# Optimization experiments

Measured on AMD Instinct MI355X. Metric: run time of the kernel, lower is better.

The kernel has to match this reference:

```python
import jax, jax.numpy as jnp
import numpy as np
import math

B, S, HID, H, DH = 4, 1024, 1024, 16, 64  # batch, seq, hidden, heads, head_dim


def _rotate_half(x):
    x1, x2 = jnp.split(x, 2, axis=-1)
    return jnp.concatenate([-x2, x1], axis=-1)


def _apply_rope(t, freqs):
    # t: [B,H,S,DH], freqs: [S,rot_dim]; here rot_dim == DH so no pass-through part
    rot = freqs.shape[-1]
    cos_ = jnp.cos(freqs)[None, None, :, :].astype(t.dtype)
    sin_ = jnp.sin(freqs)[None, None, :, :].astype(t.dtype)
    t_rot, t_pass = t[..., :rot], t[..., rot:]
    t_rot = t_rot * cos_ + _rotate_half(t_rot) * sin_
    return jnp.concatenate([t_rot, t_pass], axis=-1)


def setup_inputs() -> dict:
    key = jax.random.key(0)
    ks = jax.random.split(key, 8)
    hidden_states = jax.random.normal(ks[0], (B, S, HID), dtype=jnp.float32)
    # additive mask: valid prefix of random length per batch row, -1e9 on padding
    lengths = jax.random.randint(ks[1], (B,), 3 * S // 4, S + 1)
    pos = jnp.arange(S)
    attention_mask = jnp.where(pos[None, :] < lengths[:, None], 0.0, -1e9)
    attention_mask = attention_mask.astype(jnp.float32)[:, None, None, :]  # [B,1,1,S]
    # rotary frequencies: standard RoPE angles, duplicated halves -> [S, DH]
    inv_freq = 1.0 / (10000.0 ** (jnp.arange(0, DH // 2, dtype=jnp.float32) / (DH // 2)))
    ang = pos.astype(jnp.float32)[:, None] * inv_freq[None, :]
    freqs = jnp.concatenate([ang, ang], axis=-1)  # [S, DH]
    sc = 0.02
    Wq = jax.random.normal(ks[2], (HID, HID), dtype=jnp.float32) * sc
    Wk = jax.random.normal(ks[3], (HID, HID), dtype=jnp.float32) * sc
    Wv = jax.random.normal(ks[4], (HID, HID), dtype=jnp.float32) * sc
    bq = jnp.zeros((HID,), dtype=jnp.float32)
    bk = jnp.zeros((HID,), dtype=jnp.float32)
    bv = jnp.zeros((HID,), dtype=jnp.float32)
    return dict(hidden_states=hidden_states, attention_mask=attention_mask, freqs=freqs,
                Wq=Wq, bq=bq, Wk=Wk, bk=bk, Wv=Wv, bv=bv)


def reference(hidden_states, attention_mask, freqs, Wq, bq, Wk, bk, Wv, bv):
    b, s, _ = hidden_states.shape
    # QKV projections -> [B,H,S,DH]
    q = (hidden_states @ Wq + bq).reshape(b, s, H, DH).transpose(0, 2, 1, 3)
    k = (hidden_states @ Wk + bk).reshape(b, s, H, DH).transpose(0, 2, 1, 3)
    v = (hidden_states @ Wv + bv).reshape(b, s, H, DH).transpose(0, 2, 1, 3)
    # inline RoPE on q and k (same freqs for both, as (rotary_pos_emb,)*2)
    q = _apply_rope(q, freqs)
    k = _apply_rope(k, freqs)
    scores = jnp.einsum('bhqd,bhkd->bhqk', q, k) / math.sqrt(DH)
    scores = scores + attention_mask  # additive mask broadcast over [B,H,S,S]
    probs = jax.nn.softmax(scores, axis=-1)
    # no_prob_mask filtering: zero out masked key columns
    probs = jnp.where(attention_mask < -1e-5, 0.0, probs)
    # dropout prob is 0.0 (eval) -> identity
    ctx = jnp.einsum('bhqk,bhkd->bhqd', probs, v)
    ctx = ctx.transpose(0, 2, 1, 3).reshape(b, s, H * DH)
    return ctx
```

## Files before the change

### kernel.cpp

```cpp
#include <hip/hip_runtime.h>
#include <hip/hip_bf16.h>
#include <cmath>

#define NB   4
#define NS   1024
#define NHID 1024
#define NH   16
#define NDH  64
#define QKV_PLANE (NB * NH * NS * NDH)

typedef __attribute__((ext_vector_type(8))) short bf16x8;
typedef __attribute__((ext_vector_type(4))) float f32x4;
typedef __attribute__((ext_vector_type(8))) unsigned short u16x8;

typedef __attribute__((address_space(1))) const void gv_t;
typedef __attribute__((address_space(3))) void       lv_t;

__device__ __forceinline__ void gload16(const void* g, void* l) {
    __builtin_amdgcn_global_load_lds((gv_t*)g, (lv_t*)l, 16, 0, 0);
}

__device__ __forceinline__ unsigned short f2b(float f) {
    union { float f; unsigned int u; } v; v.f = f;
    unsigned int r = (v.u + 0x7fff + ((v.u >> 16) & 1)) >> 16;
    return (unsigned short)r;
}

__device__ __forceinline__ unsigned int f2b2(float a, float b) {
    __hip_bfloat162 h = __float22bfloat162_rn(make_float2(a, b));
    union { __hip_bfloat162 h; unsigned int u; } v; v.h = h;
    return v.u;
}

__device__ __forceinline__ float fexp2(float x) {
#if __has_builtin(__builtin_amdgcn_exp2f)
    return __builtin_amdgcn_exp2f(x);
#else
    return exp2f(x);
#endif
}

__global__ __launch_bounds__(256) void prep_kernel(
    const float* __restrict__ hs, const float* __restrict__ freqs,
    const float* __restrict__ Wq, const float* __restrict__ Wk,
    const float* __restrict__ Wv,
    unsigned short* __restrict__ hsb, unsigned short* __restrict__ wt,
    float2* __restrict__ cs)
{
    const int z   = blockIdx.z;
    const int tid = threadIdx.x;

    if (z == 3) {
        const int bx = blockIdx.y * 16 + blockIdx.x;
        #pragma unroll
        for (int c = 0; c < 16; ++c) {
            const int idx = bx * 16384 + (c * 256 + tid) * 4;
            float4 v = *(const float4*)&hs[idx];
            ushort4 o;
            o.x = f2b(v.x); o.y = f2b(v.y); o.z = f2b(v.z); o.w = f2b(v.w);
            *(ushort4*)&hsb[idx] = o;
        }
        return;
    }
    if (z == 4) {
        const int bx = blockIdx.y * 16 + blockIdx.x;
        if (bx < 128) {
            const int id = bx * 256 + tid;
            const int s = id >> 5, d = id & 31;
            const float ang = freqs[s * NDH + d];
            float sn, cn;
            sincosf(ang, &sn, &cn);
            cs[id] = make_float2(cn, sn);
        }
        return;
    }

    const float* __restrict__ W = (z == 0) ? Wq : (z == 1) ? Wk : Wv;
    __shared__ float t[64][65];
    const int k0 = blockIdx.x * 64, n0 = blockIdx.y * 64;
    #pragma unroll
    for (int c = 0; c < 16; ++c) {
        const int flat = c * 256 + tid;
        const int r = flat >> 6, cc = flat & 63;
        t[r][cc] = W[(size_t)(k0 + r) * NHID + n0 + cc];
    }
    __syncthreads();
    #pragma unroll
    for (int c = 0; c < 16; ++c) {
        const int flat = c * 256 + tid;
        const int r = flat >> 6, cc = flat & 63;
        wt[(size_t)(z * 1024 + n0 + r) * NHID + k0 + cc] = f2b(t[cc][r]);
    }
}

__global__ __launch_bounds__(256) void fused_gemm_kernel(
    const unsigned short* __restrict__ hsb,
    const unsigned short* __restrict__ wt,
    const float2* __restrict__ cs,
    const float* __restrict__ bq, const float* __restrict__ bk,
    const float* __restrict__ bv,
    unsigned short* __restrict__ qkv)
{
    __shared__ short SH[16896];
    short* As = SH;
    short* Bs = SH + 8192;

    const int tid  = threadIdx.x;
    const int lane = tid & 63;
    const int wv   = __builtin_amdgcn_readfirstlane(tid >> 6);
    const bool vmode = (blockIdx.x >= 16);

    const unsigned short* Amat;
    const unsigned short* Bmat;
    int a_base, b_base, m0, n0, vb_ = 0;
    if (!vmode) {
        n0 = blockIdx.x * 128;
        m0 = blockIdx.y * 128;
        Amat = hsb;  a_base = m0;
        Bmat = wt;   b_base = n0;
    } else {
        m0  = (blockIdx.x - 16) * 128;
        vb_ = blockIdx.y >> 3;
        n0  = (blockIdx.y & 7) * 128;
        Amat = wt;   a_base = 2048 + m0;
        Bmat = hsb;  b_base = vb_ * 1024 + n0;
    }

    const int ri  = lane >> 3;
    const int kcs = ((lane & 7) ^ ri) * 8;
    const unsigned short* gA[4];
    const unsigned short* gB[4];
    short* lA[4];
    short* lB[4];
    #pragma unroll
    for (int j = 0; j < 4; ++j) {
        const int L = 4 * wv + j;
        gA[j] = Amat + (size_t)(a_base + L * 8 + ri) * NHID + kcs;
        gB[j] = Bmat + (size_t)(b_base + L * 8 + ri) * NHID + kcs;
        lA[j] = As + L * 512;
        lB[j] = Bs + L * 512;
    }

    const int R  = (wv & 1) * 64;
    const int CW = (wv >> 1) * 64;
    const int c0 = lane & 15;
    const int g  = lane >> 4;
    const int sw7 = c0 & 7;
    int aoff[4][2], boff[4][2];
    #pragma unroll
    for (int i = 0; i < 4; ++i)
        #pragma unroll
        for (int ks = 0; ks < 2; ++ks) {
            aoff[i][ks] = (R  + 16 * i + c0) * 64 + ((g + 4 * ks) ^ sw7) * 8;
            boff[i][ks] = (CW + 16 * i + c0) * 64 + ((g + 4 * ks) ^ sw7) * 8;
        }

    f32x4 acc[4][4] = {};

    for (int k0 = 0; k0 < NHID; k0 += 64) {
        __syncthreads();
        #pragma unroll
        for (int j = 0; j < 4; ++j) {
            gload16(gA[j] + k0, lA[j]);
            gload16(gB[j] + k0, lB[j]);
        }
        __syncthreads();
        #pragma unroll
        for (int ks = 0; ks < 2; ++ks) {
            bf16x8 af[4], bfr[4];
            #pragma unroll
            for (int i = 0; i < 4; ++i) af[i]  = *(const bf16x8*)&As[aoff[i][ks]];
            #pragma unroll
            for (int j = 0; j < 4; ++j) bfr[j] = *(const bf16x8*)&Bs[boff[j][ks]];
            #pragma unroll
            for (int i = 0; i < 4; ++i)
                #pragma unroll
                for (int j = 0; j < 4; ++j)
                    acc[i][j] = __builtin_amdgcn_mfma_f32_16x16x32_bf16(
                        af[i], bfr[j], acc[i][j], 0, 0, 0);
        }
    }

    __syncthreads();
    unsigned short* E = (unsigned short*)SH;
    const int qrow4 = (lane >> 4) * 4;

    if (!vmode) {
        const int z  = n0 >> 10;
        const int hd = ((n0 & 1023) + CW) >> 6;
        const float* __restrict__ bb = (z == 0) ? bq : bk;
        const float b0 = bb[hd * 64 + c0];
        const float b1 = bb[hd * 64 + c0 + 16];
        const float b2 = bb[hd * 64 + c0 + 32];
        const float b3 = bb[hd * 64 + c0 + 48];

        #pragma unroll
        for (int i = 0; i < 4; ++i) {
            #pragma unroll
            for (int r = 0; r < 4; ++r) {
                const int ml = R + qrow4 + 16 * i + r;
                const int s  = (m0 + ml) & 1023;
                float o0 = acc[i][0][r] + b0;
                float o1 = acc[i][1][r] + b1;
                float o2 = acc[i][2][r] + b2;
                float o3 = acc[i][3][r] + b3;
                const float2 cs0 = cs[s * 32 + c0];
                const float2 cs1 = cs[s * 32 + c0 + 16];
                unsigned short* e = E + ml * 132 + CW + c0;
                e[0]  = f2b(o0 * cs0.x - o2 * cs0.y);
                e[16] = f2b(o1 * cs1.x - o3 * cs1.y);
                e[32] = f2b(o2 * cs0.x + o0 * cs0.y);
                e[48] = f2b(o3 * cs1.x + o1 * cs1.y);
            }
        }
        __syncthreads();

        const int hd0 = (n0 & 1023) >> 6;
        unsigned short* __restrict__ base = qkv + (size_t)z * QKV_PLANE;
        #pragma unroll
        for (int c = 0; c < 8; ++c) {
            const int chunk = c * 256 + tid;
            const int row   = chunk >> 4;
            const int col16 = chunk & 15;
            const int m     = m0 + row;
            const int bidx  = m >> 10;
            const int s     = m & 1023;
            const int head  = hd0 + (col16 >> 3);
            const int d     = (col16 & 7) * 8;
            u16x8 v = *(const u16x8*)&E[row * 132 + col16 * 8];
            *(u16x8*)&base[(((size_t)bidx * NH + head) * NS + s) * NDH + d] = v;
        }
    } else {
        #pragma unroll
        for (int i = 0; i < 4; ++i) {
            #pragma unroll
            for (int r = 0; r < 4; ++r) {
                const int ml  = R + qrow4 + 16 * i + r;
                const float bvm = bv[m0 + ml];
                unsigned short* e = E + ml * 132 + CW + c0;
                e[0]  = f2b(acc[i][0][r] + bvm);
                e[16] = f2b(acc[i][1][r] + bvm);
                e[32] = f2b(acc[i][2][r] + bvm);
                e[48] = f2b(acc[i][3][r] + bvm);
            }
        }
        __syncthreads();

        unsigned short* __restrict__ vplane = qkv + 2 * (size_t)QKV_PLANE;
        #pragma unroll
        for (int c = 0; c < 8; ++c) {
            const int chunk = c * 256 + tid;
            const int row   = chunk >> 4;
            const int col16 = chunk & 15;
            u16x8 v = *(const u16x8*)&E[row * 132 + col16 * 8];
            *(u16x8*)&vplane[((size_t)(vb_ * 1024 + m0 + row)) * NS
                             + n0 + col16 * 8] = v;
        }
    }
}

__global__ __launch_bounds__(512) void attn_kernel(
    const unsigned short* __restrict__ qkv, const float* __restrict__ mask,
    float* __restrict__ out)
{
    const int qt = blockIdx.x, h = blockIdx.y, b = blockIdx.z;
    const unsigned short* qp  = qkv + ((size_t)(b * NH + h) * NS) * NDH;
    const unsigned short* kp  = qp + QKV_PLANE;
    const unsigned short* vtp = qkv + 2 * (size_t)QKV_PLANE
                              + ((size_t)(b * NH + h) * NDH) * NS;

    __shared__ unsigned short KsA[64 * 64];
    __shared__ unsigned short VtA[64 * 64];
    __shared__ unsigned short PsA[128 * 64];
    __shared__ float Mk[1024];
    __shared__ float Ll[128];

    const int tid  = threadIdx.x;
    const int lane = tid & 63;
    const int w    = __builtin_amdgcn_readfirstlane(tid >> 6);
    const int c0   = lane & 15;
    const int g    = lane >> 4;
    const int sw7  = c0 & 7;
    const float C1 = 0.125f * 1.44269504f;

    {
        const int i = tid * 2;
        float2 mv = *(const float2*)&mask[(size_t)b * NS + i];
        Mk[i]     = mv.x * 1.44269504f;
        Mk[i + 1] = mv.y * 1.44269504f;
    }

    bf16x8 qf[2];
    #pragma unroll
    for (int ks = 0; ks < 2; ++ks)
        qf[ks] = *(const bf16x8*)&qp[
            (size_t)(qt * 128 + w * 16 + c0) * NDH + g * 8 + ks * 32];

    const int i8 = lane >> 3, c8 = lane & 7;
    const int gsw = (c8 ^ i8) * 8;
    const unsigned short* gk = kp  + (size_t)(w * 8 + i8) * NDH + gsw;
    const unsigned short* gv = vtp + (size_t)(w * 8 + i8) * NS  + gsw;
    unsigned short* lk = KsA + w * 512;
    unsigned short* lv = VtA + w * 512;

    int kaddr[4][2], pw4[4], pr[2];
    #pragma unroll
    for (int mt = 0; mt < 4; ++mt)
        #pragma unroll
        for (int ks = 0; ks < 2; ++ks)
            kaddr[mt][ks] = (mt * 16 + c0) * 64 + ((g + ks * 4) ^ sw7) * 8;
    #pragma unroll
    for (int mt = 0; mt < 4; ++mt)
        pw4[mt] = (w * 16 + c0) * 64 + ((2 * mt + (g >> 1)) ^ sw7) * 8 + (g & 1) * 4;
    #pragma unroll
    for (int ks = 0; ks < 2; ++ks)
        pr[ks] = (w * 16 + c0) * 64 + ((g + ks * 4) ^ sw7) * 8;

    __syncthreads();
    int ktmax = 16;
    while (ktmax > 1 && Mk[(ktmax - 1) * 64] < -1.0f) --ktmax;

    float lrow = 0.f;
    f32x4 O[4] = {};

    for (int kt = 0; kt < ktmax; ++kt) {
        __syncthreads();
        gload16(gk, lk);
        gload16(gv, lv);
        gk += 64 * NDH;
        gv += 64;
        __syncthreads();

        bf16x8 kf[4][2];
        #pragma unroll
        for (int mt = 0; mt < 4; ++mt)
            #pragma unroll
            for (int ks = 0; ks < 2; ++ks)
                kf[mt][ks] = *(const bf16x8*)&KsA[kaddr[mt][ks]];
        f32x4 S[4];
        #pragma unroll
        for (int mt = 0; mt < 4; ++mt) {
            f32x4 a = {};
            a = __builtin_amdgcn_mfma_f32_16x16x32_bf16(kf[mt][0], qf[0], a, 0, 0, 0);
            a = __builtin_amdgcn_mfma_f32_16x16x32_bf16(kf[mt][1], qf[1], a, 0, 0, 0);
            S[mt] = a;
        }

        float psum = 0.f;
        #pragma unroll
        for (int mt = 0; mt < 4; ++mt) {
            float4 mv = *(const float4*)&Mk[kt * 64 + mt * 16 + g * 4];
            float p0 = fexp2(S[mt][0] * C1 + mv.x);
            float p1 = fexp2(S[mt][1] * C1 + mv.y);
            float p2 = fexp2(S[mt][2] * C1 + mv.z);
            float p3 = fexp2(S[mt][3] * C1 + mv.w);
            psum += (p0 + p1) + (p2 + p3);
            uint2 u;
            u.x = f2b2(p0, p1);
            u.y = f2b2(p2, p3);
            *(uint2*)&PsA[pw4[mt]] = u;
        }
        lrow += psum;

        bf16x8 pf[2], vf[4][2];
        #pragma unroll
        for (int ks = 0; ks < 2; ++ks)
            pf[ks] = *(const bf16x8*)&PsA[pr[ks]];
        #pragma unroll
        for (int nd = 0; nd < 4; ++nd)
            #pragma unroll
            for (int ks = 0; ks < 2; ++ks)
                vf[nd][ks] = *(const bf16x8*)&VtA[kaddr[nd][ks]];
        #pragma unroll
        for (int nd = 0; nd < 4; ++nd) {
            f32x4 o = O[nd];
            o = __builtin_amdgcn_mfma_f32_16x16x32_bf16(pf[0], vf[nd][0], o, 0, 0, 0);
            o = __builtin_amdgcn_mfma_f32_16x16x32_bf16(pf[1], vf[nd][1], o, 0, 0, 0);
            O[nd] = o;
        }
    }

    lrow += __shfl_xor(lrow, 16);
    lrow += __shfl_xor(lrow, 32);
    if (g == 0) Ll[w * 16 + c0] = lrow;
    float4 lv4 = *(const float4*)&Ll[w * 16 + g * 4];
    float inv[4];
    #pragma unroll
    for (int r = 0; r < 4; ++r) inv[r] = 1.0f / ((const float*)&lv4)[r];

    #pragma unroll
    for (int nd = 0; nd < 4; ++nd)
        #pragma unroll
        for (int r = 0; r < 4; ++r) {
            const int row = qt * 128 + w * 16 + g * 4 + r;
            const int col = h * 64 + nd * 16 + c0;
            out[((size_t)b * NS + row) * NHID + col] = O[nd][r] * inv[r];
        }
}

extern "C" void kernel_launch(void* const* d_in, const int* in_sizes, int n_in,
                              void* d_out, int out_size, void* d_ws, size_t ws_size,
                              hipStream_t stream) {
    const float* hs    = (const float*)d_in[0];
    const float* mask  = (const float*)d_in[1];
    const float* freqs = (const float*)d_in[2];
    const float* Wq    = (const float*)d_in[3];
    const float* bq    = (const float*)d_in[4];
    const float* Wk    = (const float*)d_in[5];
    const float* bk    = (const float*)d_in[6];
    const float* Wv    = (const float*)d_in[7];
    const float* bv    = (const float*)d_in[8];
    float* out = (float*)d_out;

    char* ws = (char*)d_ws;
    unsigned short* qkvb = (unsigned short*)ws;
    unsigned short* hsb  = (unsigned short*)(ws + 25165824);
    unsigned short* wtb  = (unsigned short*)(ws + 33554432);
    float2*         csb  = (float2*)       (ws + 39845888);

    prep_kernel<<<dim3(16, 16, 5), 256, 0, stream>>>(hs, freqs, Wq, Wk, Wv,
                                                     hsb, wtb, csb);
    fused_gemm_kernel<<<dim3(24, 32), 256, 0, stream>>>(hsb, wtb, csb,
                                                        bq, bk, bv, qkvb);
    attn_kernel<<<dim3(NS / 128, NH, NB), 512, 0, stream>>>(qkvb, mask, out);
}
```

Before: 156.9 us.

## Double-buffer LDS tiles in QKV GEMM and attention, halve attention block size

```diff
diff --git a/kernel.cpp b/kernel.cpp
--- a/kernel.cpp
+++ b/kernel.cpp
@@ -102,8 +102,6 @@
     unsigned short* __restrict__ qkv)
 {
     __shared__ short SH[16896];
-    short* As = SH;
-    short* Bs = SH + 8192;
 
     const int tid  = threadIdx.x;
     const int lane = tid & 63;
@@ -126,62 +124,66 @@
         Bmat = hsb;  b_base = vb_ * 1024 + n0;
     }
 
-    const int ri  = lane >> 3;
-    const int kcs = ((lane & 7) ^ ri) * 8;
-    const unsigned short* gA[4];
-    const unsigned short* gB[4];
-    short* lA[4];
-    short* lB[4];
-    #pragma unroll
-    for (int j = 0; j < 4; ++j) {
-        const int L = 4 * wv + j;
-        gA[j] = Amat + (size_t)(a_base + L * 8 + ri) * NHID + kcs;
-        gB[j] = Bmat + (size_t)(b_base + L * 8 + ri) * NHID + kcs;
-        lA[j] = As + L * 512;
-        lB[j] = Bs + L * 512;
+    const int ri  = lane >> 2;
+    const int kcs = (((lane & 3) ^ ((lane >> 3) & 3))) * 8;
+    const unsigned short* gA[2];
+    const unsigned short* gB[2];
+    int lAo[2], lBo[2];
+    #pragma unroll
+    for (int j = 0; j < 2; ++j) {
+        const int L = 2 * wv + j;
+        gA[j] = Amat + (size_t)(a_base + L * 16 + ri) * NHID + kcs;
+        gB[j] = Bmat + (size_t)(b_base + L * 16 + ri) * NHID + kcs;
+        lAo[j] = L * 512;
+        lBo[j] = 8192 + L * 512;
     }
 
     const int R  = (wv & 1) * 64;
     const int CW = (wv >> 1) * 64;
     const int c0 = lane & 15;
     const int g  = lane >> 4;
-    const int sw7 = c0 & 7;
-    int aoff[4][2], boff[4][2];
-    #pragma unroll
-    for (int i = 0; i < 4; ++i)
-        #pragma unroll
-        for (int ks = 0; ks < 2; ++ks) {
-            aoff[i][ks] = (R  + 16 * i + c0) * 64 + ((g + 4 * ks) ^ sw7) * 8;
-            boff[i][ks] = (CW + 16 * i + c0) * 64 + ((g + 4 * ks) ^ sw7) * 8;
-        }
+    const int swz = (g ^ ((c0 >> 1) & 3)) * 8;
+    int aoff[4], boff[4];
+    #pragma unroll
+    for (int i = 0; i < 4; ++i) {
+        aoff[i] = (R  + 16 * i + c0) * 32 + swz;
+        boff[i] = 8192 + (CW + 16 * i + c0) * 32 + swz;
+    }
 
     f32x4 acc[4][4] = {};
 
-    for (int k0 = 0; k0 < NHID; k0 += 64) {
+    #pragma unroll
+    for (int j = 0; j < 2; ++j) {
+        gload16(gA[j], SH + lAo[j]);
+        gload16(gB[j], SH + lBo[j]);
+    }
+    __syncthreads();
+
+    for (int it = 0; it < 32; ++it) {
+        const int cur = (it & 1) * 4096;
+        if (it + 1 < 32) {
+            const int nxt = ((it + 1) & 1) * 4096;
+            const int ko  = (it + 1) * 32;
+            #pragma unroll
+            for (int j = 0; j < 2; ++j) {
+                gload16(gA[j] + ko, SH + nxt + lAo[j]);
+                gload16(gB[j] + ko, SH + nxt + lBo[j]);
+            }
+        }
+        bf16x8 af[4], bfr[4];
+        #pragma unroll
+        for (int i = 0; i < 4; ++i) af[i]  = *(const bf16x8*)&SH[cur + aoff[i]];
+        #pragma unroll
+        for (int j = 0; j < 4; ++j) bfr[j] = *(const bf16x8*)&SH[cur + boff[j]];
+        #pragma unroll
+        for (int i = 0; i < 4; ++i)
+            #pragma unroll
+            for (int j = 0; j < 4; ++j)
+                acc[i][j] = __builtin_amdgcn_mfma_f32_16x16x32_bf16(
+                    af[i], bfr[j], acc[i][j], 0, 0, 0);
         __syncthreads();
-        #pragma unroll
-        for (int j = 0; j < 4; ++j) {
-            gload16(gA[j] + k0, lA[j]);
-            gload16(gB[j] + k0, lB[j]);
-        }
-        __syncthreads();
-        #pragma unroll
-        for (int ks = 0; ks < 2; ++ks) {
-            bf16x8 af[4], bfr[4];
-            #pragma unroll
-            for (int i = 0; i < 4; ++i) af[i]  = *(const bf16x8*)&As[aoff[i][ks]];
-            #pragma unroll
-            for (int j = 0; j < 4; ++j) bfr[j] = *(const bf16x8*)&Bs[boff[j][ks]];
-            #pragma unroll
-            for (int i = 0; i < 4; ++i)
-                #pragma unroll
-                for (int j = 0; j < 4; ++j)
-                    acc[i][j] = __builtin_amdgcn_mfma_f32_16x16x32_bf16(
-                        af[i], bfr[j], acc[i][j], 0, 0, 0);
-        }
-    }
-
-    __syncthreads();
+    }
+
     unsigned short* E = (unsigned short*)SH;
     const int qrow4 = (lane >> 4) * 4;
 
@@ -259,7 +261,7 @@
     }
 }
 
-__global__ __launch_bounds__(512) void attn_kernel(
+__global__ __launch_bounds__(256) void attn_kernel(
     const unsigned short* __restrict__ qkv, const float* __restrict__ mask,
     float* __restrict__ out)
 {
@@ -269,8 +271,8 @@
     const unsigned short* vtp = qkv + 2 * (size_t)QKV_PLANE
                               + ((size_t)(b * NH + h) * NDH) * NS;
 
-    __shared__ unsigned short KsA[64 * 64];
-    __shared__ unsigned short VtA[64 * 64];
+    __shared__ unsigned short KsA[2 * 4096];
+    __shared__ unsigned short VtA[2 * 4096];
     __shared__ unsigned short PsA[128 * 64];
     __shared__ float Mk[1024];
     __shared__ float Ll[128];
@@ -283,119 +285,160 @@
     const int sw7  = c0 & 7;
     const float C1 = 0.125f * 1.44269504f;
 
+    const int i8 = lane >> 3, c8 = lane & 7;
+    const int gsw = (c8 ^ i8) * 8;
+    const unsigned short* gk[2];
+    const unsigned short* gv[2];
+    int lko[2], lvo[2];
+    #pragma unroll
+    for (int j = 0; j < 2; ++j) {
+        const int L = 2 * w + j;
+        gk[j] = kp  + (size_t)(L * 8 + i8) * NDH + gsw;
+        gv[j] = vtp + (size_t)(L * 8 + i8) * NS  + gsw;
+        lko[j] = L * 512;
+        lvo[j] = L * 512;
+    }
+
+    #pragma unroll
+    for (int j = 0; j < 2; ++j) {
+        gload16(gk[j], KsA + lko[j]);
+        gload16(gv[j], VtA + lvo[j]);
+    }
+
     {
-        const int i = tid * 2;
-        float2 mv = *(const float2*)&mask[(size_t)b * NS + i];
+        const int i = tid * 4;
+        float4 mv = *(const float4*)&mask[(size_t)b * NS + i];
         Mk[i]     = mv.x * 1.44269504f;
         Mk[i + 1] = mv.y * 1.44269504f;
-    }
-
-    bf16x8 qf[2];
-    #pragma unroll
-    for (int ks = 0; ks < 2; ++ks)
-        qf[ks] = *(const bf16x8*)&qp[
-            (size_t)(qt * 128 + w * 16 + c0) * NDH + g * 8 + ks * 32];
-
-    const int i8 = lane >> 3, c8 = lane & 7;
-    const int gsw = (c8 ^ i8) * 8;
-    const unsigned short* gk = kp  + (size_t)(w * 8 + i8) * NDH + gsw;
-    const unsigned short* gv = vtp + (size_t)(w * 8 + i8) * NS  + gsw;
-    unsigned short* lk = KsA + w * 512;
-    unsigned short* lv = VtA + w * 512;
-
-    int kaddr[4][2], pw4[4], pr[2];
+        Mk[i + 2] = mv.z * 1.44269504f;
+        Mk[i + 3] = mv.w * 1.44269504f;
+    }
+
+    bf16x8 qf[2][2];
+    #pragma unroll
+    for (int nt = 0; nt < 2; ++nt)
+        #pragma unroll
+        for (int ks = 0; ks < 2; ++ks)
+            qf[nt][ks] = *(const bf16x8*)&qp[
+                (size_t)(qt * 128 + w * 32 + nt * 16 + c0) * NDH + g * 8 + ks * 32];
+
+    int kaddr[4][2], pw[2][4], pr[2][2];
     #pragma unroll
     for (int mt = 0; mt < 4; ++mt)
         #pragma unroll
         for (int ks = 0; ks < 2; ++ks)
             kaddr[mt][ks] = (mt * 16 + c0) * 64 + ((g + ks * 4) ^ sw7) * 8;
     #pragma unroll
-    for (int mt = 0; mt < 4; ++mt)
-        pw4[mt] = (w * 16 + c0) * 64 + ((2 * mt + (g >> 1)) ^ sw7) * 8 + (g & 1) * 4;
-    #pragma unroll
-    for (int ks = 0; ks < 2; ++ks)
-        pr[ks] = (w * 16 + c0) * 64 + ((g + ks * 4) ^ sw7) * 8;
+    for (int nt = 0; nt < 2; ++nt)
+        #pragma unroll
+        for (int mt = 0; mt < 4; ++mt)
+            pw[nt][mt] = (w * 32 + nt * 16 + c0) * 64
+                       + ((2 * mt + (g >> 1)) ^ sw7) * 8 + (g & 1) * 4;
+    #pragma unroll
+    for (int mt = 0; mt < 2; ++mt)
+        #pragma unroll
+        for (int ks = 0; ks < 2; ++ks)
+            pr[mt][ks] = (w * 32 + mt * 16 + c0) * 64 + ((g + ks * 4) ^ sw7) * 8;
 
     __syncthreads();
+
     int ktmax = 16;
     while (ktmax > 1 && Mk[(ktmax - 1) * 64] < -1.0f) --ktmax;
 
-    float lrow = 0.f;
-    f32x4 O[4] = {};
+    float lrow[2] = { 0.f, 0.f };
+    f32x4 O[2][4] = {};
 
     for (int kt = 0; kt < ktmax; ++kt) {
+        const int cur = (kt & 1) * 4096;
+        if (kt + 1 < ktmax) {
+            const int nxt = ((kt + 1) & 1) * 4096;
+            const size_t ko = (size_t)(kt + 1) * 64;
+            #pragma unroll
+            for (int j = 0; j < 2; ++j) {
+                gload16(gk[j] + ko * NDH, KsA + nxt + lko[j]);
+                gload16(gv[j] + ko,       VtA + nxt + lvo[j]);
+            }
+        }
+
+        bf16x8 kf[4][2];
+        #pragma unroll
+        for (int mt = 0; mt < 4; ++mt)
+            #pragma unroll
+            for (int ks = 0; ks < 2; ++ks)
+                kf[mt][ks] = *(const bf16x8*)&KsA[cur + kaddr[mt][ks]];
+
+        #pragma unroll
+        for (int nt = 0; nt < 2; ++nt) {
+            f32x4 S[4];
+            #pragma unroll
+            for (int mt = 0; mt < 4; ++mt) {
+                f32x4 a = {};
+                a = __builtin_amdgcn_mfma_f32_16x16x32_bf16(kf[mt][0], qf[nt][0], a, 0, 0, 0);
+                a = __builtin_amdgcn_mfma_f32_16x16x32_bf16(kf[mt][1], qf[nt][1], a, 0, 0, 0);
+                S[mt] = a;
+            }
+            float psum = 0.f;
+            #pragma unroll
+            for (int mt = 0; mt < 4; ++mt) {
+                float4 mv = *(const float4*)&Mk[kt * 64 + mt * 16 + g * 4];
+                float p0 = fexp2(S[mt][0] * C1 + mv.x);
+                float p1 = fexp2(S[mt][1] * C1 + mv.y);
+                float p2 = fexp2(S[mt][2] * C1 + mv.z);
+                float p3 = fexp2(S[mt][3] * C1 + mv.w);
+                psum += (p0 + p1) + (p2 + p3);
+                uint2 u;
+                u.x = f2b2(p0, p1);
+                u.y = f2b2(p2, p3);
+                *(uint2*)&PsA[pw[nt][mt]] = u;
+            }
+            lrow[nt] += psum;
+        }
+
+        bf16x8 pf[2][2], vf[4][2];
+        #pragma unroll
+        for (int mt = 0; mt < 2; ++mt)
+            #pragma unroll
+            for (int ks = 0; ks < 2; ++ks)
+                pf[mt][ks] = *(const bf16x8*)&PsA[pr[mt][ks]];
+        #pragma unroll
+        for (int nd = 0; nd < 4; ++nd)
+            #pragma unroll
+            for (int ks = 0; ks < 2; ++ks)
+                vf[nd][ks] = *(const bf16x8*)&VtA[cur + kaddr[nd][ks]];
+        #pragma unroll
+        for (int mt = 0; mt < 2; ++mt)
+            #pragma unroll
+            for (int nd = 0; nd < 4; ++nd) {
+                f32x4 o = O[mt][nd];
+                o = __builtin_amdgcn_mfma_f32_16x16x32_bf16(pf[mt][0], vf[nd][0], o, 0, 0, 0);
+                o = __builtin_amdgcn_mfma_f32_16x16x32_bf16(pf[mt][1], vf[nd][1], o, 0, 0, 0);
+                O[mt][nd] = o;
+            }
+
         __syncthreads();
-        gload16(gk, lk);
-        gload16(gv, lv);
-        gk += 64 * NDH;
-        gv += 64;
-        __syncthreads();
-
-        bf16x8 kf[4][2];
-        #pragma unroll
-        for (int mt = 0; mt < 4; ++mt)
-            #pragma unroll
-            for (int ks = 0; ks < 2; ++ks)
-                kf[mt][ks] = *(const bf16x8*)&KsA[kaddr[mt][ks]];
-        f32x4 S[4];
-        #pragma unroll
-        for (int mt = 0; mt < 4; ++mt) {
-            f32x4 a = {};
-            a = __builtin_amdgcn_mfma_f32_16x16x32_bf16(kf[mt][0], qf[0], a, 0, 0, 0);
-            a = __builtin_amdgcn_mfma_f32_16x16x32_bf16(kf[mt][1], qf[1], a, 0, 0, 0);
-            S[mt] = a;
-        }
-
-        float psum = 0.f;
-        #pragma unroll
-        for (int mt = 0; mt < 4; ++mt) {
-            float4 mv = *(const float4*)&Mk[kt * 64 + mt * 16 + g * 4];
-            float p0 = fexp2(S[mt][0] * C1 + mv.x);
-            float p1 = fexp2(S[mt][1] * C1 + mv.y);
-            float p2 = fexp2(S[mt][2] * C1 + mv.z);
-            float p3 = fexp2(S[mt][3] * C1 + mv.w);
-            psum += (p0 + p1) + (p2 + p3);
-            uint2 u;
-            u.x = f2b2(p0, p1);
-            u.y = f2b2(p2, p3);
-            *(uint2*)&PsA[pw4[mt]] = u;
-        }
-        lrow += psum;
-
-        bf16x8 pf[2], vf[4][2];
-        #pragma unroll
-        for (int ks = 0; ks < 2; ++ks)
-            pf[ks] = *(const bf16x8*)&PsA[pr[ks]];
+    }
+
+    #pragma unroll
+    for (int nt = 0; nt < 2; ++nt) {
+        lrow[nt] += __shfl_xor(lrow[nt], 16);
+        lrow[nt] += __shfl_xor(lrow[nt], 32);
+        if (g == 0) Ll[w * 32 + nt * 16 + c0] = lrow[nt];
+    }
+    #pragma unroll
+    for (int mt = 0; mt < 2; ++mt) {
+        float4 lv4 = *(const float4*)&Ll[w * 32 + mt * 16 + g * 4];
+        float inv[4];
+        #pragma unroll
+        for (int r = 0; r < 4; ++r) inv[r] = 1.0f / ((const float*)&lv4)[r];
         #pragma unroll
         for (int nd = 0; nd < 4; ++nd)
             #pragma unroll
-            for (int ks = 0; ks < 2; ++ks)
-                vf[nd][ks] = *(const bf16x8*)&VtA[kaddr[nd][ks]];
-        #pragma unroll
-        for (int nd = 0; nd < 4; ++nd) {
-            f32x4 o = O[nd];
-            o = __builtin_amdgcn_mfma_f32_16x16x32_bf16(pf[0], vf[nd][0], o, 0, 0, 0);
-            o = __builtin_amdgcn_mfma_f32_16x16x32_bf16(pf[1], vf[nd][1], o, 0, 0, 0);
-            O[nd] = o;
-        }
-    }
-
-    lrow += __shfl_xor(lrow, 16);
-    lrow += __shfl_xor(lrow, 32);
-    if (g == 0) Ll[w * 16 + c0] = lrow;
-    float4 lv4 = *(const float4*)&Ll[w * 16 + g * 4];
-    float inv[4];
-    #pragma unroll
-    for (int r = 0; r < 4; ++r) inv[r] = 1.0f / ((const float*)&lv4)[r];
-
-    #pragma unroll
-    for (int nd = 0; nd < 4; ++nd)
-        #pragma unroll
-        for (int r = 0; r < 4; ++r) {
-            const int row = qt * 128 + w * 16 + g * 4 + r;
-            const int col = h * 64 + nd * 16 + c0;
-            out[((size_t)b * NS + row) * NHID + col] = O[nd][r] * inv[r];
-        }
+            for (int r = 0; r < 4; ++r) {
+                const int row = qt * 128 + w * 32 + mt * 16 + g * 4 + r;
+                const int col = h * 64 + nd * 16 + c0;
+                out[((size_t)b * NS + row) * NHID + col] = O[mt][nd][r] * inv[r];
+            }
+    }
 }
 
 extern "C" void kernel_launch(void* const* d_in, const int* in_sizes, int n_in,
@@ -422,5 +465,5 @@
                                                      hsb, wtb, csb);
     fused_gemm_kernel<<<dim3(24, 32), 256, 0, stream>>>(hsb, wtb, csb,
                                                         bq, bk, bv, qkvb);
-    attn_kernel<<<dim3(NS / 128, NH, NB), 512, 0, stream>>>(qkvb, mask, out);
-}
+    attn_kernel<<<dim3(NS / 128, NH, NB), 256, 0, stream>>>(qkvb, mask, out);
+}
```

Result: slower. 164.2 us (+4.6%).
